# Kernel tuning notes

Hardware: AMD Instinct MI355X
Metric: run time of the kernel (lower is better)

The kernel has to match this reference:

```python
import jax, jax.numpy as jnp
import numpy as np

TEX_H = 256
TEX_W = 256
F_CH = 16
D_FACTOR = 0.5
DECAY = float(np.sqrt(2.0 * D_FACTOR * D_FACTOR))           # sqrt(d^2 + d^2)
AF = int(-np.log(0.1) * DECAY + 0.5)                        # active_field = 2
K = 2 * AF                                                  # 4x4 splat window


def setup_inputs() -> dict:
    key = jax.random.key(0)
    k1, k2, k3 = jax.random.split(key, 3)
    B, H, W = 8, 256, 256
    f_map = jax.random.normal(k1, (B, H, W, F_CH), dtype=jnp.float32)
    uv_map = jax.random.uniform(k2, (B, H, W, 2), dtype=jnp.float32)   # uv in [0,1)
    mask = (jax.random.uniform(k3, (B, H, W, 1)) < 0.5).astype(jnp.float32)
    return {"f_map": f_map, "uv_map": uv_map, "mask": mask}


def reference(f_map, uv_map, mask):
    B, H, W, C = f_map.shape
    N = B * H * W
    # uv_map[..., ::-1] * [tex_h, tex_w]: v comes from channel 1, u from channel 0
    v = (uv_map[..., 1] * TEX_H).reshape(N)
    u = (uv_map[..., 0] * TEX_W).reshape(N)
    pix = f_map.reshape(N, C)
    m = mask.reshape(N)  # 1 = masked pixel contributes (TF gathers where mask==1)

    v_shift = jnp.maximum(v - AF, 0.0)
    u_shift = jnp.maximum(u - AF, 0.0)
    offs = jnp.arange(K, dtype=jnp.float32)
    v_grid = v_shift[:, None, None] + offs[None, :, None]   # [N,K,K]
    u_grid = u_shift[:, None, None] + offs[None, None, :]   # [N,K,K]

    du = jnp.abs(u_grid - u[:, None, None])
    du = jnp.minimum(du, jnp.abs(du - TEX_W))               # wrap-around distance
    dv = jnp.abs(v_grid - v[:, None, None])
    dv = jnp.minimum(dv, jnp.abs(dv - TEX_H))
    wmap = jnp.exp(-jnp.sqrt(du * du + dv * dv) / DECAY)
    wmap = wmap * (wmap > 0.1) * m[:, None, None]           # threshold + mask gating

    vi = v_grid.astype(jnp.int32)
    ui = u_grid.astype(jnp.int32)
    valid = (vi < TEX_H) & (ui < TEX_W)                     # drop out-of-range splats
    wmap = wmap * valid
    idx = (jnp.clip(vi, 0, TEX_H - 1) * TEX_W + jnp.clip(ui, 0, TEX_W - 1)).reshape(-1)

    w_flat = wmap.reshape(-1)                               # [N*K*K]
    vals = (wmap.reshape(N, K * K)[..., None] * pix[:, None, :]).reshape(-1, C)

    wsum = jnp.zeros((TEX_H * TEX_W,), jnp.float32).at[idx].add(w_flat)
    csum = jnp.zeros((TEX_H * TEX_W, C), jnp.float32).at[idx].add(vals)
    wsum = wsum.reshape(TEX_H, TEX_W, 1)
    csum = csum.reshape(TEX_H, TEX_W, C)

    tex = (csum * (wsum > 0.01)) / (wsum + 0.001)           # weighted average
    return jnp.broadcast_to(tex[None], (B, TEX_H, TEX_W, C))
```

## Files before the change

### kernel.cpp

```cpp
#include <hip/hip_runtime.h>

#define TEX_H 256
#define TEX_W 256
#define FCH 16
#define NPIX (8 * 256 * 256)
#define NCELL (256 * 256)
#define CAP 16

#define SQRT2_F 1.41421356237f
#define W_EDGE   0.24311673443f
#define W_DIAG   0.13533528324f

#define HALO_C_OFF 0
#define HALO_N_OFF (NCELL * 16)
#define DIR_C_OFF  (HALO_N_OFF + NCELL)
#define DIR_W_OFF  (DIR_C_OFF + 2 * 4 * 256 * 16)
#define CNT_OFF    (DIR_W_OFF + 2 * 4 * 256)
#define ENT_OFF    (CNT_OFF + NCELL)
#define WS_FLOATS  (ENT_OFF + NCELL * CAP)
#define ZERO_FLOATS ENT_OFF

__device__ __forceinline__ void boundary_splat(float u, float v, float f, int c,
                                               float* __restrict__ ws) {
    float us = fmaxf(u - 2.0f, 0.0f);
    float vs = fmaxf(v - 2.0f, 0.0f);
    #pragma unroll
    for (int kv = 0; kv < 4; ++kv) {
        float vg = vs + (float)kv;
        int vi = (int)vg;
        float dvf = fabsf(vg - v);
        #pragma unroll
        for (int ku = 0; ku < 4; ++ku) {
            float ug = us + (float)ku;
            int ui = (int)ug;
            float duf = fabsf(ug - u);
            float w = expf(-sqrtf(duf * duf + dvf * dvf) * SQRT2_F);
            if (w > 0.1f && vi < TEX_H && ui < TEX_W) {
                int cell = (ui < 4) ? (ui * 256 + vi)
                                    : ((4 + vi) * 256 + ui);
                unsafeAtomicAdd(&ws[DIR_C_OFF + cell * FCH + c], w * f);
                if (c == 0) unsafeAtomicAdd(&ws[DIR_W_OFF + cell], w);
            }
        }
    }
}

__global__ __launch_bounds__(256) void bin_kernel(
    const float*  __restrict__ f_map,
    const float2* __restrict__ uv_map,
    const float*  __restrict__ mask,
    float* __restrict__ ws)
{
    int tid = blockIdx.x * 256 + threadIdx.x;
    int pix = tid >> 4;
    int c   = tid & 15;

    if (mask[pix] == 0.0f) return;

    float2 uv = uv_map[pix];
    float u = uv.x * 256.0f;
    float v = uv.y * 256.0f;

    if (u >= 2.0f && v >= 2.0f) {
        int cell = ((int)v) * 256 + (int)u;
        int slot = 0;
        if (c == 0) slot = atomicAdd((int*)ws + CNT_OFF + cell, 1);
        slot = __shfl(slot, 0, 16);
        if (slot < CAP) {
            if (c == 0) ((unsigned*)ws)[ENT_OFF + cell * CAP + slot] = (unsigned)pix;
        } else {
            float f = f_map[pix * FCH + c];
            unsafeAtomicAdd(&ws[HALO_C_OFF + cell * FCH + c], f);
            if (c == 0) unsafeAtomicAdd(&ws[HALO_N_OFF + cell], 1.0f);
        }
    } else {
        float f = f_map[pix * FCH + c];
        boundary_splat(u, v, f, c, ws);
    }
}

__global__ __launch_bounds__(256) void gather_kernel(
    const float* __restrict__ f_map,
    float* __restrict__ ws)
{
    int tid  = blockIdx.x * 256 + threadIdx.x;
    int cell = tid >> 4;
    int c    = tid & 15;

    int cnt = min(((const int*)ws)[CNT_OFF + cell], CAP);
    if (cnt == 0) return;

    unsigned ent = ((const unsigned*)ws)[ENT_OFF + cell * CAP + c];
    float acc = 0.0f;

    int e = 0;
    for (; e + 4 <= cnt; e += 4) {
        unsigned p0 = __shfl(ent, e + 0, 16);
        unsigned p1 = __shfl(ent, e + 1, 16);
        unsigned p2 = __shfl(ent, e + 2, 16);
        unsigned p3 = __shfl(ent, e + 3, 16);
        float f0 = f_map[p0 * FCH + c];
        float f1 = f_map[p1 * FCH + c];
        float f2 = f_map[p2 * FCH + c];
        float f3 = f_map[p3 * FCH + c];
        acc += f0; acc += f1; acc += f2; acc += f3;
    }
    for (; e < cnt; ++e) {
        unsigned p = __shfl(ent, e, 16);
        acc += f_map[p * FCH + c];
    }

    unsafeAtomicAdd(&ws[HALO_C_OFF + cell * FCH + c], acc);
    if (c == 0) unsafeAtomicAdd(&ws[HALO_N_OFF + cell], (float)cnt);
}

__global__ __launch_bounds__(256) void splat_kernel(
    const float*  __restrict__ f_map,
    const float2* __restrict__ uv_map,
    const float*  __restrict__ mask,
    float* __restrict__ ws)
{
    int tid = blockIdx.x * 256 + threadIdx.x;
    int pix = tid >> 4;
    int c   = tid & 15;

    if (mask[pix] == 0.0f) return;

    float2 uv = uv_map[pix];
    float u = uv.x * 256.0f;
    float v = uv.y * 256.0f;
    float f = f_map[pix * FCH + c];

    if (u >= 2.0f && v >= 2.0f) {
        int cell = ((int)v) * 256 + (int)u;
        unsafeAtomicAdd(&ws[HALO_C_OFF + cell * FCH + c], f);
        if (c == 0) unsafeAtomicAdd(&ws[HALO_N_OFF + cell], 1.0f);
    } else {
        boundary_splat(u, v, f, c, ws);
    }
}

__global__ __launch_bounds__(256) void finalize_kernel(
    const float* __restrict__ ws,
    float* __restrict__ out)
{
    int tile = blockIdx.x;
    int r0 = (tile >> 5) << 3;
    int c0 = (tile & 31) << 3;
    int tx = threadIdx.x >> 2;
    int c4 = threadIdx.x & 3;
    int gr = r0 + (tx >> 3);
    int gc = c0 + (tx & 7);

    float4 cs = make_float4(0.f, 0.f, 0.f, 0.f);
    float wsm = 0.0f;

    #pragma unroll
    for (int a = -1; a <= 1; ++a) {
        int cr = gr + a;
        if (cr < 0 || cr > 255) continue;
        #pragma unroll
        for (int b = -1; b <= 1; ++b) {
            int cc = gc + b;
            if (cc < 0 || cc > 255) continue;
            float w = (a == 0 && b == 0) ? 1.0f
                    : ((a == 0 || b == 0) ? W_EDGE : W_DIAG);
            int cell = cr * 256 + cc;
            float4 h = *(const float4*)&ws[HALO_C_OFF + cell * FCH + c4 * 4];
            cs.x += w * h.x; cs.y += w * h.y; cs.z += w * h.z; cs.w += w * h.w;
            wsm  += w * ws[HALO_N_OFF + cell];
        }
    }

    if (gc < 4) {
        int cell = gc * 256 + gr;
        float4 d = *(const float4*)&ws[DIR_C_OFF + cell * FCH + c4 * 4];
        cs.x += d.x; cs.y += d.y; cs.z += d.z; cs.w += d.w;
        wsm  += ws[DIR_W_OFF + cell];
    } else if (gr < 4) {
        int cell = (4 + gr) * 256 + gc;
        float4 d = *(const float4*)&ws[DIR_C_OFF + cell * FCH + c4 * 4];
        cs.x += d.x; cs.y += d.y; cs.z += d.z; cs.w += d.w;
        wsm  += ws[DIR_W_OFF + cell];
    }

    float s = (wsm > 0.01f) ? (1.0f / (wsm + 0.001f)) : 0.0f;
    cs.x *= s; cs.y *= s; cs.z *= s; cs.w *= s;

    size_t base = ((size_t)gr * 256 + gc) * FCH + c4 * 4;
    #pragma unroll
    for (int b = 0; b < 8; ++b) {
        *(float4*)&out[(size_t)b * (256 * 256 * FCH) + base] = cs;
    }
}

extern "C" void kernel_launch(void* const* d_in, const int* in_sizes, int n_in,
                              void* d_out, int out_size, void* d_ws, size_t ws_size,
                              hipStream_t stream) {
    const float*  f_map  = (const float*)d_in[0];
    const float2* uv_map = (const float2*)d_in[1];
    const float*  mask   = (const float*)d_in[2];
    float* out = (float*)d_out;
    float* ws  = (float*)d_ws;

    bool bucketed = ws_size >= (size_t)WS_FLOATS * sizeof(float);

    if (bucketed) {
        hipMemsetAsync(ws, 0, (size_t)ZERO_FLOATS * sizeof(float), stream);
        bin_kernel<<<(NPIX * 16) / 256, 256, 0, stream>>>(f_map, uv_map, mask, ws);
        gather_kernel<<<(NCELL * 16) / 256, 256, 0, stream>>>(f_map, ws);
    } else {
        hipMemsetAsync(ws, 0, (size_t)CNT_OFF * sizeof(float), stream);
        splat_kernel<<<(NPIX * 16) / 256, 256, 0, stream>>>(f_map, uv_map, mask, ws);
    }
    finalize_kernel<<<1024, 256, 0, stream>>>(ws, out);
}
```

Measured before the change: 65.02 us.

## Use one thread per pixel in binning, direct-store gather, nontemporal output stores

The binning kernel now maps one thread per pixel instead of sixteen threads per pixel. This cuts the launched threads by 16x and removes the shuffle, while overflow and boundary pixels load their 16 channels as vectors and issue 16 atomics from one thread. The gather kernel writes plain stores for cells at or under capacity instead of atomics. The finalize kernel uses nontemporal stores for the 8x-broadcast output. The risk is serialized atomic work per thread on boundary and overflow pixels, and less memory-level parallelism in the binning pass.

```diff
diff --git a/kernel.cpp b/kernel.cpp
--- a/kernel.cpp
+++ b/kernel.cpp
@@ -10,6 +10,8 @@
 #define SQRT2_F 1.41421356237f
 #define W_EDGE   0.24311673443f
 #define W_DIAG   0.13533528324f
+
+typedef float vf4 __attribute__((ext_vector_type(4)));
 
 #define HALO_C_OFF 0
 #define HALO_N_OFF (NCELL * 16)
@@ -20,16 +22,32 @@
 #define WS_FLOATS  (ENT_OFF + NCELL * CAP)
 #define ZERO_FLOATS ENT_OFF
 
-__device__ __forceinline__ void boundary_splat(float u, float v, float f, int c,
-                                               float* __restrict__ ws) {
+__device__ __forceinline__ void load16(const float* __restrict__ src, float* dst) {
+    vf4 a = *(const vf4*)(src + 0);
+    vf4 b = *(const vf4*)(src + 4);
+    vf4 c = *(const vf4*)(src + 8);
+    vf4 d = *(const vf4*)(src + 12);
+    dst[0]=a.x; dst[1]=a.y; dst[2]=a.z; dst[3]=a.w;
+    dst[4]=b.x; dst[5]=b.y; dst[6]=b.z; dst[7]=b.w;
+    dst[8]=c.x; dst[9]=c.y; dst[10]=c.z; dst[11]=c.w;
+    dst[12]=d.x; dst[13]=d.y; dst[14]=d.z; dst[15]=d.w;
+}
+
+__device__ __forceinline__ void add16(float* __restrict__ base, float w,
+                                      const float* __restrict__ fv) {
+    #pragma unroll
+    for (int i = 0; i < 16; ++i) unsafeAtomicAdd(base + i, w * fv[i]);
+}
+
+__device__ __forceinline__ void boundary_splat16(float u, float v,
+                                                 const float* __restrict__ fv,
+                                                 float* __restrict__ ws) {
     float us = fmaxf(u - 2.0f, 0.0f);
     float vs = fmaxf(v - 2.0f, 0.0f);
-    #pragma unroll
     for (int kv = 0; kv < 4; ++kv) {
         float vg = vs + (float)kv;
         int vi = (int)vg;
         float dvf = fabsf(vg - v);
-        #pragma unroll
         for (int ku = 0; ku < 4; ++ku) {
             float ug = us + (float)ku;
             int ui = (int)ug;
@@ -38,8 +56,8 @@
             if (w > 0.1f && vi < TEX_H && ui < TEX_W) {
                 int cell = (ui < 4) ? (ui * 256 + vi)
                                     : ((4 + vi) * 256 + ui);
-                unsafeAtomicAdd(&ws[DIR_C_OFF + cell * FCH + c], w * f);
-                if (c == 0) unsafeAtomicAdd(&ws[DIR_W_OFF + cell], w);
+                add16(ws + DIR_C_OFF + (size_t)cell * FCH, w, fv);
+                unsafeAtomicAdd(ws + DIR_W_OFF + cell, w);
             }
         }
     }
@@ -51,10 +69,7 @@
     const float*  __restrict__ mask,
     float* __restrict__ ws)
 {
-    int tid = blockIdx.x * 256 + threadIdx.x;
-    int pix = tid >> 4;
-    int c   = tid & 15;
-
+    int pix = blockIdx.x * 256 + threadIdx.x;
     if (mask[pix] == 0.0f) return;
 
     float2 uv = uv_map[pix];
@@ -63,19 +78,19 @@
 
     if (u >= 2.0f && v >= 2.0f) {
         int cell = ((int)v) * 256 + (int)u;
-        int slot = 0;
-        if (c == 0) slot = atomicAdd((int*)ws + CNT_OFF + cell, 1);
-        slot = __shfl(slot, 0, 16);
+        int slot = atomicAdd((int*)ws + CNT_OFF + cell, 1);
         if (slot < CAP) {
-            if (c == 0) ((unsigned*)ws)[ENT_OFF + cell * CAP + slot] = (unsigned)pix;
+            ((unsigned*)ws)[ENT_OFF + cell * CAP + slot] = (unsigned)pix;
         } else {
-            float f = f_map[pix * FCH + c];
-            unsafeAtomicAdd(&ws[HALO_C_OFF + cell * FCH + c], f);
-            if (c == 0) unsafeAtomicAdd(&ws[HALO_N_OFF + cell], 1.0f);
-        }
-    } else {
-        float f = f_map[pix * FCH + c];
-        boundary_splat(u, v, f, c, ws);
+            float fv[16];
+            load16(f_map + (size_t)pix * FCH, fv);
+            add16(ws + HALO_C_OFF + (size_t)cell * FCH, 1.0f, fv);
+            unsafeAtomicAdd(ws + HALO_N_OFF + cell, 1.0f);
+        }
+    } else {
+        float fv[16];
+        load16(f_map + (size_t)pix * FCH, fv);
+        boundary_splat16(u, v, fv, ws);
     }
 }
 
@@ -87,31 +102,37 @@
     int cell = tid >> 4;
     int c    = tid & 15;
 
-    int cnt = min(((const int*)ws)[CNT_OFF + cell], CAP);
+    int cnt = ((const int*)ws)[CNT_OFF + cell];
     if (cnt == 0) return;
+    int n = min(cnt, CAP);
 
     unsigned ent = ((const unsigned*)ws)[ENT_OFF + cell * CAP + c];
     float acc = 0.0f;
 
     int e = 0;
-    for (; e + 4 <= cnt; e += 4) {
+    for (; e + 4 <= n; e += 4) {
         unsigned p0 = __shfl(ent, e + 0, 16);
         unsigned p1 = __shfl(ent, e + 1, 16);
         unsigned p2 = __shfl(ent, e + 2, 16);
         unsigned p3 = __shfl(ent, e + 3, 16);
-        float f0 = f_map[p0 * FCH + c];
-        float f1 = f_map[p1 * FCH + c];
-        float f2 = f_map[p2 * FCH + c];
-        float f3 = f_map[p3 * FCH + c];
+        float f0 = f_map[(size_t)p0 * FCH + c];
+        float f1 = f_map[(size_t)p1 * FCH + c];
+        float f2 = f_map[(size_t)p2 * FCH + c];
+        float f3 = f_map[(size_t)p3 * FCH + c];
         acc += f0; acc += f1; acc += f2; acc += f3;
     }
-    for (; e < cnt; ++e) {
+    for (; e < n; ++e) {
         unsigned p = __shfl(ent, e, 16);
-        acc += f_map[p * FCH + c];
-    }
-
-    unsafeAtomicAdd(&ws[HALO_C_OFF + cell * FCH + c], acc);
-    if (c == 0) unsafeAtomicAdd(&ws[HALO_N_OFF + cell], (float)cnt);
+        acc += f_map[(size_t)p * FCH + c];
+    }
+
+    if (cnt <= CAP) {
+        ws[HALO_C_OFF + (size_t)cell * FCH + c] = acc;
+        if (c == 0) ws[HALO_N_OFF + cell] = (float)cnt;
+    } else {
+        unsafeAtomicAdd(&ws[HALO_C_OFF + (size_t)cell * FCH + c], acc);
+        if (c == 0) unsafeAtomicAdd(&ws[HALO_N_OFF + cell], (float)n);
+    }
 }
 
 __global__ __launch_bounds__(256) void splat_kernel(
@@ -133,10 +154,30 @@
 
     if (u >= 2.0f && v >= 2.0f) {
         int cell = ((int)v) * 256 + (int)u;
-        unsafeAtomicAdd(&ws[HALO_C_OFF + cell * FCH + c], f);
+        unsafeAtomicAdd(&ws[HALO_C_OFF + (size_t)cell * FCH + c], f);
         if (c == 0) unsafeAtomicAdd(&ws[HALO_N_OFF + cell], 1.0f);
     } else {
-        boundary_splat(u, v, f, c, ws);
+        float us = fmaxf(u - 2.0f, 0.0f);
+        float vs = fmaxf(v - 2.0f, 0.0f);
+        #pragma unroll
+        for (int kv = 0; kv < 4; ++kv) {
+            float vg = vs + (float)kv;
+            int vi = (int)vg;
+            float dvf = fabsf(vg - v);
+            #pragma unroll
+            for (int ku = 0; ku < 4; ++ku) {
+                float ug = us + (float)ku;
+                int ui = (int)ug;
+                float duf = fabsf(ug - u);
+                float w = expf(-sqrtf(duf * duf + dvf * dvf) * SQRT2_F);
+                if (w > 0.1f && vi < TEX_H && ui < TEX_W) {
+                    int cell = (ui < 4) ? (ui * 256 + vi)
+                                        : ((4 + vi) * 256 + ui);
+                    unsafeAtomicAdd(&ws[DIR_C_OFF + (size_t)cell * FCH + c], w * f);
+                    if (c == 0) unsafeAtomicAdd(&ws[DIR_W_OFF + cell], w);
+                }
+            }
+        }
     }
 }
 
@@ -152,7 +193,7 @@
     int gr = r0 + (tx >> 3);
     int gc = c0 + (tx & 7);
 
-    float4 cs = make_float4(0.f, 0.f, 0.f, 0.f);
+    vf4 cs = {0.f, 0.f, 0.f, 0.f};
     float wsm = 0.0f;
 
     #pragma unroll
@@ -166,31 +207,29 @@
             float w = (a == 0 && b == 0) ? 1.0f
                     : ((a == 0 || b == 0) ? W_EDGE : W_DIAG);
             int cell = cr * 256 + cc;
-            float4 h = *(const float4*)&ws[HALO_C_OFF + cell * FCH + c4 * 4];
-            cs.x += w * h.x; cs.y += w * h.y; cs.z += w * h.z; cs.w += w * h.w;
-            wsm  += w * ws[HALO_N_OFF + cell];
+            vf4 h = *(const vf4*)&ws[HALO_C_OFF + (size_t)cell * FCH + c4 * 4];
+            cs += w * h;
+            wsm += w * ws[HALO_N_OFF + cell];
         }
     }
 
     if (gc < 4) {
         int cell = gc * 256 + gr;
-        float4 d = *(const float4*)&ws[DIR_C_OFF + cell * FCH + c4 * 4];
-        cs.x += d.x; cs.y += d.y; cs.z += d.z; cs.w += d.w;
-        wsm  += ws[DIR_W_OFF + cell];
+        cs += *(const vf4*)&ws[DIR_C_OFF + (size_t)cell * FCH + c4 * 4];
+        wsm += ws[DIR_W_OFF + cell];
     } else if (gr < 4) {
         int cell = (4 + gr) * 256 + gc;
-        float4 d = *(const float4*)&ws[DIR_C_OFF + cell * FCH + c4 * 4];
-        cs.x += d.x; cs.y += d.y; cs.z += d.z; cs.w += d.w;
-        wsm  += ws[DIR_W_OFF + cell];
+        cs += *(const vf4*)&ws[DIR_C_OFF + (size_t)cell * FCH + c4 * 4];
+        wsm += ws[DIR_W_OFF + cell];
     }
 
     float s = (wsm > 0.01f) ? (1.0f / (wsm + 0.001f)) : 0.0f;
-    cs.x *= s; cs.y *= s; cs.z *= s; cs.w *= s;
+    cs *= s;
 
     size_t base = ((size_t)gr * 256 + gc) * FCH + c4 * 4;
     #pragma unroll
     for (int b = 0; b < 8; ++b) {
-        *(float4*)&out[(size_t)b * (256 * 256 * FCH) + base] = cs;
+        __builtin_nontemporal_store(cs, (vf4*)&out[(size_t)b * (256 * 256 * FCH) + base]);
     }
 }
 
@@ -206,11 +245,11 @@
     bool bucketed = ws_size >= (size_t)WS_FLOATS * sizeof(float);
 
     if (bucketed) {
-        hipMemsetAsync(ws, 0, (size_t)ZERO_FLOATS * sizeof(float), stream);
-        bin_kernel<<<(NPIX * 16) / 256, 256, 0, stream>>>(f_map, uv_map, mask, ws);
+        (void)hipMemsetAsync(ws, 0, (size_t)ZERO_FLOATS * sizeof(float), stream);
+        bin_kernel<<<NPIX / 256, 256, 0, stream>>>(f_map, uv_map, mask, ws);
         gather_kernel<<<(NCELL * 16) / 256, 256, 0, stream>>>(f_map, ws);
     } else {
-        hipMemsetAsync(ws, 0, (size_t)CNT_OFF * sizeof(float), stream);
+        (void)hipMemsetAsync(ws, 0, (size_t)CNT_OFF * sizeof(float), stream);
         splat_kernel<<<(NPIX * 16) / 256, 256, 0, stream>>>(f_map, uv_map, mask, ws);
     }
     finalize_kernel<<<1024, 256, 0, stream>>>(ws, out);
```

Measured after the change: 86.62 us. 1.33x slower.
